# Kernel tuning notes

Measured on AMD Instinct MI355X. Metric: run time of the kernel, lower is better.

The kernel has to match this reference:

```python
import jax, jax.numpy as jnp
import numpy as np
import math

FACTOR = 1

def setup_inputs() -> dict:
    key = jax.random.key(0)
    kq, kk, kv = jax.random.split(key, 3)
    B, L, H, D = 8, 4096, 8, 32
    queries = jax.random.normal(kq, (B, L, H, D), dtype=jnp.float32)
    keys = jax.random.normal(kk, (B, L, H, D), dtype=jnp.float32)
    values = jax.random.normal(kv, (B, L, H, D), dtype=jnp.float32)
    return {"queries": queries, "keys": keys, "values": values}


def reference(queries, keys, values):
    # queries/keys/values: [B, L, H, D]
    B, L, H, D = queries.shape
    q = jnp.transpose(queries, (0, 2, 1, 3))  # [B,H,L,D]
    k = jnp.transpose(keys, (0, 2, 1, 3))
    v = jnp.transpose(values, (0, 2, 1, 3))

    # FFT-based cross-correlation (period-based dependency discovery)
    q_fft = jnp.fft.rfft(q, axis=2)
    k_fft = jnp.fft.rfft(k, axis=2)
    spd = jnp.sum(q_fft * jnp.conj(k_fft), axis=-1)      # [B,H,Lf]
    corr = jnp.fft.irfft(spd, n=L, axis=-1)              # [B,H,L]

    # Time-delay aggregation (inference path: per-sample delays)
    top_k = max(1, min(int(FACTOR * math.log(L)), L))
    weights, delays = jax.lax.top_k(corr, top_k)          # [B,H,K]
    weights = jax.nn.softmax(weights, axis=-1)

    # roll values by -delay via circular gather: pattern[l] = v[(l+delay) % L]
    init_index = jnp.arange(L)[None, None, None, :]       # [1,1,1,L]
    idx = (init_index + delays[..., None]) % L            # [B,H,K,L]
    patterns = jnp.take_along_axis(v[:, :, None, :, :], idx[..., None], axis=3)  # [B,H,K,L,D]
    agg = jnp.sum(patterns * weights[..., None, None], axis=2)  # [B,H,L,D]

    # dropout is identity in eval mode
    return jnp.transpose(agg, (0, 2, 1, 3))  # [B,L,H,D]
```

## Files before the change

kernel.cpp:

```cpp
#include <hip/hip_runtime.h>
#include <hip/hip_bf16.h>


#define SWZ(i) ((i) ^ (((i) >> 4) & 15))
#define SLICE 2056

typedef float nfloat4 __attribute__((ext_vector_type(4)));

__device__ inline void cmul(float& outr, float& outi, float ar, float ai, float br, float bi) {
    outr = ar * br - ai * bi;
    outi = ar * bi + ai * br;
}

template<int DIR>
__device__ inline void fft16(float* vr, float* vi) {
    const float C1 = 0.92387953251128675613f;
    const float S1 = 0.38268343236508977173f;
    const float R2 = 0.70710678118654752440f;
    float ur[16], ui[16];
#pragma unroll
    for (int n2 = 0; n2 < 4; ++n2) {
        float ar = vr[n2],      ai = vi[n2];
        float br = vr[n2 + 4],  bi = vi[n2 + 4];
        float cr = vr[n2 + 8],  ci = vi[n2 + 8];
        float dr = vr[n2 + 12], di = vi[n2 + 12];
        float acr = ar + cr, aci = ai + ci;
        float asr = ar - cr, asi = ai - ci;
        float bdr = br + dr, bdi = bi + di;
        float bsr = br - dr, bsi = bi - di;
        ur[0 + n2]  = acr + bdr; ui[0 + n2]  = aci + bdi;
        ur[8 + n2]  = acr - bdr; ui[8 + n2]  = aci - bdi;
        if (DIR < 0) {
            ur[4 + n2]  = asr + bsi; ui[4 + n2]  = asi - bsr;
            ur[12 + n2] = asr - bsi; ui[12 + n2] = asi + bsr;
        } else {
            ur[4 + n2]  = asr - bsi; ui[4 + n2]  = asi + bsr;
            ur[12 + n2] = asr + bsi; ui[12 + n2] = asi - bsr;
        }
    }
#pragma unroll
    for (int k1 = 1; k1 < 4; ++k1) {
#pragma unroll
        for (int n2 = 1; n2 < 4; ++n2) {
            int e = k1 * n2;
            float c, s;
            if (e == 1)      { c = C1;  s = S1; }
            else if (e == 2) { c = R2;  s = R2; }
            else if (e == 3) { c = S1;  s = C1; }
            else if (e == 4) { c = 0.f; s = 1.f; }
            else if (e == 6) { c = -R2; s = R2; }
            else             { c = -C1; s = -S1; }
            int idx = k1 * 4 + n2;
            float r0 = ur[idx], i0 = ui[idx];
            if (DIR < 0) { ur[idx] = r0 * c + i0 * s; ui[idx] = i0 * c - r0 * s; }
            else         { ur[idx] = r0 * c - i0 * s; ui[idx] = i0 * c + r0 * s; }
        }
    }
#pragma unroll
    for (int k1 = 0; k1 < 4; ++k1) {
        float ar = ur[k1 * 4 + 0], ai = ui[k1 * 4 + 0];
        float br = ur[k1 * 4 + 1], bi = ui[k1 * 4 + 1];
        float cr = ur[k1 * 4 + 2], ci = ui[k1 * 4 + 2];
        float dr = ur[k1 * 4 + 3], di = ui[k1 * 4 + 3];
        float acr = ar + cr, aci = ai + ci;
        float asr = ar - cr, asi = ai - ci;
        float bdr = br + dr, bdi = bi + di;
        float bsr = br - dr, bsi = bi - di;
        vr[k1]      = acr + bdr; vi[k1]      = aci + bdi;
        vr[k1 + 8]  = acr - bdr; vi[k1 + 8]  = aci - bdi;
        if (DIR < 0) {
            vr[k1 + 4]  = asr + bsi; vi[k1 + 4]  = asi - bsr;
            vr[k1 + 12] = asr - bsi; vi[k1 + 12] = asi + bsr;
        } else {
            vr[k1 + 4]  = asr - bsi; vi[k1 + 4]  = asi + bsr;
            vr[k1 + 12] = asr + bsi; vi[k1 + 12] = asi - bsr;
        }
    }
}

template<int DIR, int NS>
__device__ inline void fft_pass16_ip(float2* __restrict__ buf,
                                     float w1r, float w1i, int j) {
    float vr[16], vi[16];
#pragma unroll
    for (int r = 0; r < 16; ++r) {
        float2 x = buf[SWZ(j + r * 256)];
        vr[r] = x.x; vi[r] = x.y;
    }
    if (NS > 1) {
        float wr[16], wi[16];
        wr[1] = w1r; wi[1] = w1i;
#pragma unroll
        for (int r = 2; r < 16; ++r)
            cmul(wr[r], wi[r], wr[r >> 1], wi[r >> 1], wr[(r + 1) >> 1], wi[(r + 1) >> 1]);
#pragma unroll
        for (int r = 1; r < 16; ++r) {
            float r0 = vr[r], i0 = vi[r];
            vr[r] = r0 * wr[r] - i0 * wi[r];
            vi[r] = r0 * wi[r] + i0 * wr[r];
        }
    }
    fft16<DIR>(vr, vi);
    __syncthreads();
    int base = (j / NS) * (16 * NS) + (j & (NS - 1));
#pragma unroll
    for (int r = 0; r < 16; ++r)
        buf[SWZ(base + r * NS)] = make_float2(vr[r], vi[r]);
}

template<int DIR>
__device__ inline void fft4096_ip(float2* buf, float c2, float s2,
                                  float c3, float s3, int tid) {
    fft_pass16_ip<DIR, 1>(buf, 1.f, 0.f, tid);  __syncthreads();
    fft_pass16_ip<DIR, 16>(buf, c2, s2, tid);   __syncthreads();
    fft_pass16_ip<DIR, 256>(buf, c3, s3, tid);  __syncthreads();
}

__global__ __launch_bounds__(256) void transpose_pack_kernel(const float4* __restrict__ q4,
                                                             const float4* __restrict__ k4,
                                                             float4* __restrict__ xT4) {
    __shared__ float qs[64][65];
    __shared__ float ks[64][65];
    int bid = blockIdx.x;
    int ct = bid & 3;
    int lt = (bid >> 2) & 63;
    int b  = bid >> 8;
    int tid = threadIdx.x;
    int l0 = lt * 64, c0 = ct * 64;
    int cw = tid & 15;
    int rr = tid >> 4;
#pragma unroll
    for (int it = 0; it < 4; ++it) {
        int row = it * 16 + rr;
        size_t g = (size_t)(b * 4096 + l0 + row) * 64u + (size_t)(c0 / 4 + cw);
        float4 qv = q4[g];
        float4 kv = k4[g];
        qs[row][cw * 4 + 0] = qv.x; qs[row][cw * 4 + 1] = qv.y;
        qs[row][cw * 4 + 2] = qv.z; qs[row][cw * 4 + 3] = qv.w;
        ks[row][cw * 4 + 0] = kv.x; ks[row][cw * 4 + 1] = kv.y;
        ks[row][cw * 4 + 2] = kv.z; ks[row][cw * 4 + 3] = kv.w;
    }
    __syncthreads();
    int a = tid & 31;
    int cb = tid >> 5;
#pragma unroll
    for (int it = 0; it < 8; ++it) {
        int cc = it * 8 + cb;
        float4 o;
        o.x = qs[2 * a][cc];     o.y = ks[2 * a][cc];
        o.z = qs[2 * a + 1][cc]; o.w = ks[2 * a + 1][cc];
        xT4[(size_t)(b * 256 + c0 + cc) * 2048u + (size_t)(l0 / 2 + a)] = o;
    }
}

__device__ inline void spd_pair_accum(const float2* A, float4* acc, float& accny, int tid) {
#pragma unroll
    for (int t = 0; t < 4; ++t) {
        int f0 = 2 * tid + 512 * t;
        float2 za = A[SWZ(f0)];
        float2 zb = A[SWZ(f0 + 1)];
        float2 ma = A[SWZ((4096 - f0) & 4095)];
        float2 mb = A[SWZ(4095 - f0)];
        float qr = za.x + ma.x, qi = za.y - ma.y;
        float kr = za.y + ma.y, ki = za.x - ma.x;
        acc[t].x += 0.25f * (qr * kr - qi * ki);
        acc[t].y += 0.25f * (qr * ki + qi * kr);
        qr = zb.x + mb.x; qi = zb.y - mb.y;
        kr = zb.y + mb.y; ki = zb.x - mb.x;
        acc[t].z += 0.25f * (qr * kr - qi * ki);
        acc[t].w += 0.25f * (qr * ki + qi * kr);
    }
    float2 zn = A[SWZ(2048)];
    accny += zn.x * zn.y;
}

__global__ __launch_bounds__(256, 4) void fwd_spd_fast(const float2* __restrict__ xT,
                                                       float2* __restrict__ spd_d) {
    __shared__ float2 A[4096];
    int bid = blockIdx.x;
    int tid = threadIdx.x;
    int b = bid >> 7, p = bid & 127;
    const float TWO_PI = 6.2831853071795864769f;
    float ang2 = TWO_PI * (float)((tid & 15) * 16) * (1.0f / 4096.0f);
    float ang3 = TWO_PI * (float)tid * (1.0f / 4096.0f);
    float c2 = cosf(ang2), s2 = sinf(ang2);
    float c3 = cosf(ang3), s3 = sinf(ang3);
    float4 acc[4];
#pragma unroll
    for (int t = 0; t < 4; ++t) acc[t] = make_float4(0.f, 0.f, 0.f, 0.f);
    float accny = 0.f;
#pragma unroll
    for (int cc = 0; cc < 2; ++cc) {
        if (cc) __syncthreads();
        const float4* src4 = (const float4*)(xT + (size_t)(b * 256 + p * 2 + cc) * 4096u);
#pragma unroll
        for (int t = 0; t < 8; ++t) {
            float4 x = src4[tid + t * 256];
            int n = 2 * (tid + t * 256);
            A[SWZ(n)]     = make_float2(x.x, x.y);
            A[SWZ(n + 1)] = make_float2(x.z, x.w);
        }
        __syncthreads();
        fft4096_ip<-1>(A, c2, -s2, c3, -s3, tid);
        spd_pair_accum(A, acc, accny, tid);
    }
    float4* dst4 = (float4*)(spd_d + (size_t)bid * SLICE);
#pragma unroll
    for (int t = 0; t < 4; ++t) dst4[tid + t * 256] = acc[t];
    if (tid == 0) spd_d[(size_t)bid * SLICE + 2048] = make_float2(accny, 0.f);
}

__global__ __launch_bounds__(256, 4) void fwd_spd_slow(const float* __restrict__ q,
                                                       const float* __restrict__ k,
                                                       float2* __restrict__ spd_d) {
    __shared__ float2 A[4096];
    int bid = blockIdx.x;
    int tid = threadIdx.x;
    int b = bid >> 7, p = bid & 127;
    const float TWO_PI = 6.2831853071795864769f;
    float ang2 = TWO_PI * (float)((tid & 15) * 16) * (1.0f / 4096.0f);
    float ang3 = TWO_PI * (float)tid * (1.0f / 4096.0f);
    float c2 = cosf(ang2), s2 = sinf(ang2);
    float c3 = cosf(ang3), s3 = sinf(ang3);
    float4 acc[4];
#pragma unroll
    for (int t = 0; t < 4; ++t) acc[t] = make_float4(0.f, 0.f, 0.f, 0.f);
    float accny = 0.f;
#pragma unroll
    for (int cc = 0; cc < 2; ++cc) {
        if (cc) __syncthreads();
        size_t base = (size_t)b * 1048576u + (size_t)(p * 2 + cc);
#pragma unroll
        for (int t = 0; t < 16; ++t) {
            int n = tid + t * 256;
            A[SWZ(n)] = make_float2(q[base + (size_t)n * 256u], k[base + (size_t)n * 256u]);
        }
        __syncthreads();
        fft4096_ip<-1>(A, c2, -s2, c3, -s3, tid);
        spd_pair_accum(A, acc, accny, tid);
    }
    float4* dst4 = (float4*)(spd_d + (size_t)bid * SLICE);
#pragma unroll
    for (int t = 0; t < 4; ++t) dst4[tid + t * 256] = acc[t];
    if (tid == 0) spd_d[(size_t)bid * SLICE + 2048] = make_float2(accny, 0.f);
}

__global__ __launch_bounds__(256, 4) void ifft_topk_kernel(const float2* __restrict__ spd_d,
                                                           float* __restrict__ wout,
                                                           int* __restrict__ dout) {
    __shared__ float2 A[4096];
    __shared__ float rv[8][4];
    __shared__ int   ri[8][4];
    int bh = blockIdx.x;
    int b = bh >> 3, h = bh & 7;
    int tid = threadIdx.x;
    const float TWO_PI = 6.2831853071795864769f;
    float ang2 = TWO_PI * (float)((tid & 15) * 16) * (1.0f / 4096.0f);
    float ang3 = TWO_PI * (float)tid * (1.0f / 4096.0f);
    float c2 = cosf(ang2), s2 = sinf(ang2);
    float c3 = cosf(ang3), s3 = sinf(ang3);
    const float sc = 1.0f / 4096.0f;
    const float2* base = spd_d + (size_t)(b * 128 + h * 16) * SLICE;
    const float4* base4 = (const float4*)base;
#pragma unroll
    for (int t = 0; t < 4; ++t) {
        int f0 = 2 * tid + 512 * t;
        float4 a = make_float4(0.f, 0.f, 0.f, 0.f);
#pragma unroll
        for (int s = 0; s < 16; ++s) {
            float4 x = base4[(size_t)s * (SLICE / 2) + (size_t)(tid + 256 * t)];
            a.x += x.x; a.y += x.y; a.z += x.z; a.w += x.w;
        }
        float r0 = a.x * sc, i0 = a.y * sc;
        float r1 = a.z * sc, i1 = a.w * sc;
        A[SWZ(f0)]     = make_float2(r0, i0);
        A[SWZ(f0 + 1)] = make_float2(r1, i1);
        if (f0 > 0) A[SWZ(4096 - f0)] = make_float2(r0, -i0);
        A[SWZ(4095 - f0)] = make_float2(r1, -i1);
    }
    if (tid == 0) {
        float ny = 0.f;
#pragma unroll
        for (int s = 0; s < 16; ++s) ny += base[(size_t)s * SLICE + 2048].x;
        A[SWZ(2048)] = make_float2(ny * sc, 0.f);
    }
    __syncthreads();
    fft4096_ip<1>(A, c2, s2, c3, s3, tid);
    float cv[16];
#pragma unroll
    for (int t = 0; t < 16; ++t) cv[t] = A[SWZ(tid + t * 256)].x;

    int lane = tid & 63, wid = tid >> 6;
    float topv[8]; int topi[8];
    for (int kk = 0; kk < 8; ++kk) {
        float best = -3.0e38f; int bi = 0;
#pragma unroll
        for (int t = 0; t < 16; ++t) {
            int f = tid + t * 256;
            if (cv[t] > best) { best = cv[t]; bi = f; }
        }
#pragma unroll
        for (int off = 32; off > 0; off >>= 1) {
            float ov = __shfl_xor(best, off, 64);
            int   oi = __shfl_xor(bi, off, 64);
            if (ov > best || (ov == best && oi < bi)) { best = ov; bi = oi; }
        }
        if (lane == 0) { rv[kk][wid] = best; ri[kk][wid] = bi; }
        __syncthreads();
        float fb = rv[kk][0]; int fi = ri[kk][0];
#pragma unroll
        for (int w = 1; w < 4; ++w) {
            float ov = rv[kk][w]; int oi = ri[kk][w];
            if (ov > fb || (ov == fb && oi < fi)) { fb = ov; fi = oi; }
        }
        topv[kk] = fb; topi[kk] = fi;
        if (tid == (fi & 255)) {
            int t_owner = fi >> 8;
#pragma unroll
            for (int t = 0; t < 16; ++t)
                if (t == t_owner) cv[t] = -3.0e38f;
        }
    }
    if (tid == 0) {
        float mx = topv[0];
        float e[8], s = 0.0f;
#pragma unroll
        for (int kk = 0; kk < 8; ++kk) { e[kk] = expf(topv[kk] - mx); s += e[kk]; }
        float inv = 1.0f / s;
#pragma unroll
        for (int kk = 0; kk < 8; ++kk) {
            wout[bh * 8 + kk] = e[kk] * inv;
            dout[bh * 8 + kk] = topi[kk];
        }
    }
}

__global__ __launch_bounds__(256) void agg_kernel(const float4* __restrict__ v4,
                                                  const float* __restrict__ w,
                                                  const int* __restrict__ dl,
                                                  float4* __restrict__ out4) {
    __shared__ float sw[64];
    __shared__ int   sd[64];
    int blk = blockIdx.x;
    int b = blk & 7, lg = blk >> 3;
    int tid = threadIdx.x;
    if (tid < 64) {
        int h = tid >> 3, kk = tid & 7;
        sw[tid] = w[(b * 8 + h) * 8 + kk];
        sd[tid] = dl[(b * 8 + h) * 8 + kk];
    }
    __syncthreads();
    int lq = tid >> 6;
    int c4 = tid & 63;
    int h  = c4 >> 3;
    float w_[8]; int d_[8];
#pragma unroll
    for (int kk = 0; kk < 8; ++kk) { w_[kk] = sw[h * 8 + kk]; d_[kk] = sd[h * 8 + kk]; }
#pragma unroll
    for (int rep = 0; rep < 4; ++rep) {
        int l = lg * 16 + rep * 4 + lq;
        float4 acc = make_float4(0.f, 0.f, 0.f, 0.f);
#pragma unroll
        for (int kk = 0; kk < 8; ++kk) {
            int l2 = (l + d_[kk]) & 4095;
            float4 x = v4[(size_t)(b * 4096 + l2) * 64u + (size_t)c4];
            acc.x += w_[kk] * x.x; acc.y += w_[kk] * x.y;
            acc.z += w_[kk] * x.z; acc.w += w_[kk] * x.w;
        }
        nfloat4 nv = {acc.x, acc.y, acc.z, acc.w};
        __builtin_nontemporal_store(nv,
            (nfloat4*)&out4[(size_t)(b * 4096 + l) * 64u + (size_t)c4]);
    }
}

extern "C" void kernel_launch(void* const* d_in, const int* in_sizes, int n_in,
                              void* d_out, int out_size, void* d_ws, size_t ws_size,
                              hipStream_t stream) {
    const float* q = (const float*)d_in[0];
    const float* k = (const float*)d_in[1];
    const float* v = (const float*)d_in[2];
    float* ws  = (float*)d_ws;
    float2* spd_d = (float2*)d_out;

    const size_t XT_FLOATS = 16777216u;
    const size_t FAST_FLOATS = XT_FLOATS + 1024u;
    bool fast = ws_size >= FAST_FLOATS * sizeof(float);

    if (fast) {
        float* wbuf = ws + XT_FLOATS;
        int*   dbuf = (int*)(wbuf + 512);
        transpose_pack_kernel<<<2048, 256, 0, stream>>>((const float4*)q, (const float4*)k,
                                                        (float4*)ws);
        fwd_spd_fast<<<1024, 256, 0, stream>>>((const float2*)ws, spd_d);
        ifft_topk_kernel<<<64, 256, 0, stream>>>(spd_d, wbuf, dbuf);
        agg_kernel<<<2048, 256, 0, stream>>>((const float4*)v, wbuf, dbuf, (float4*)d_out);
    } else {
        float* wbuf = ws;
        int*   dbuf = (int*)(wbuf + 512);
        fwd_spd_slow<<<1024, 256, 0, stream>>>(q, k, spd_d);
        ifft_topk_kernel<<<64, 256, 0, stream>>>(spd_d, wbuf, dbuf);
        agg_kernel<<<2048, 256, 0, stream>>>((const float4*)v, wbuf, dbuf, (float4*)d_out);
    }
}
```

Measured before the change: 95.28 us.

## Fuse first radix-16 FFT pass into transpose kernel

The transpose kernel now gathers strided time samples (stride 256) for each channel, performs the first radix-16 FFT stage in registers, and writes the partially transformed data. The SPD kernel then runs only the remaining two FFT passes, saving one LDS pass and a barrier per 4096-point transform. Occupancy hint for the SPD kernel is raised from 4 to 5 blocks per CU. The transpose kernel's global reads become more scattered across L, and its writes now depend on the FFT pass matching the expected in-place ordering.

```diff
diff --git a/kernel.cpp b/kernel.cpp
--- a/kernel.cpp
+++ b/kernel.cpp
@@ -116,41 +116,51 @@
     fft_pass16_ip<DIR, 256>(buf, c3, s3, tid);  __syncthreads();
 }
 
-__global__ __launch_bounds__(256) void transpose_pack_kernel(const float4* __restrict__ q4,
+template<int DIR>
+__device__ inline void fft4096_p23(float2* buf, float c2, float s2,
+                                   float c3, float s3, int tid) {
+    fft_pass16_ip<DIR, 16>(buf, c2, s2, tid);   __syncthreads();
+    fft_pass16_ip<DIR, 256>(buf, c3, s3, tid);  __syncthreads();
+}
+
+__global__ __launch_bounds__(256) void transpose_fft1_kernel(const float4* __restrict__ q4,
                                                              const float4* __restrict__ k4,
-                                                             float4* __restrict__ xT4) {
-    __shared__ float qs[64][65];
-    __shared__ float ks[64][65];
+                                                             float4* __restrict__ y4) {
+    __shared__ float2 X[64][65];
     int bid = blockIdx.x;
-    int ct = bid & 3;
-    int lt = (bid >> 2) & 63;
+    int jt = bid & 63;
+    int ct = (bid >> 6) & 3;
     int b  = bid >> 8;
     int tid = threadIdx.x;
-    int l0 = lt * 64, c0 = ct * 64;
+    int j0 = jt * 4, c0 = ct * 64;
     int cw = tid & 15;
-    int rr = tid >> 4;
+    int rb = tid >> 4;
 #pragma unroll
     for (int it = 0; it < 4; ++it) {
-        int row = it * 16 + rr;
-        size_t g = (size_t)(b * 4096 + l0 + row) * 64u + (size_t)(c0 / 4 + cw);
+        int rr = it * 16 + rb;
+        int l  = j0 + (rr & 3) + 256 * (rr >> 2);
+        size_t g = (size_t)(b * 4096 + l) * 64u + (size_t)(c0 / 4 + cw);
         float4 qv = q4[g];
         float4 kv = k4[g];
-        qs[row][cw * 4 + 0] = qv.x; qs[row][cw * 4 + 1] = qv.y;
-        qs[row][cw * 4 + 2] = qv.z; qs[row][cw * 4 + 3] = qv.w;
-        ks[row][cw * 4 + 0] = kv.x; ks[row][cw * 4 + 1] = kv.y;
-        ks[row][cw * 4 + 2] = kv.z; ks[row][cw * 4 + 3] = kv.w;
+        X[rr][cw * 4 + 0] = make_float2(qv.x, kv.x);
+        X[rr][cw * 4 + 1] = make_float2(qv.y, kv.y);
+        X[rr][cw * 4 + 2] = make_float2(qv.z, kv.z);
+        X[rr][cw * 4 + 3] = make_float2(qv.w, kv.w);
     }
     __syncthreads();
-    int a = tid & 31;
-    int cb = tid >> 5;
-#pragma unroll
-    for (int it = 0; it < 8; ++it) {
-        int cc = it * 8 + cb;
-        float4 o;
-        o.x = qs[2 * a][cc];     o.y = ks[2 * a][cc];
-        o.z = qs[2 * a + 1][cc]; o.w = ks[2 * a + 1][cc];
-        xT4[(size_t)(b * 256 + c0 + cc) * 2048u + (size_t)(l0 / 2 + a)] = o;
-    }
+    int cc = tid & 63;
+    int jj = tid >> 6;
+    float vr[16], vi[16];
+#pragma unroll
+    for (int t = 0; t < 16; ++t) {
+        float2 x = X[t * 4 + jj][cc];
+        vr[t] = x.x; vi[t] = x.y;
+    }
+    fft16<-1>(vr, vi);
+    float4* dst = y4 + (size_t)(b * 256 + c0 + cc) * 2048u + (size_t)(j0 + jj) * 8u;
+#pragma unroll
+    for (int p = 0; p < 8; ++p)
+        dst[p] = make_float4(vr[2 * p], vi[2 * p], vr[2 * p + 1], vi[2 * p + 1]);
 }
 
 __device__ inline void spd_pair_accum(const float2* A, float4* acc, float& accny, int tid) {
@@ -174,7 +184,7 @@
     accny += zn.x * zn.y;
 }
 
-__global__ __launch_bounds__(256, 4) void fwd_spd_fast(const float2* __restrict__ xT,
+__global__ __launch_bounds__(256, 5) void fwd_spd_fast(const float2* __restrict__ y,
                                                        float2* __restrict__ spd_d) {
     __shared__ float2 A[4096];
     int bid = blockIdx.x;
@@ -192,7 +202,7 @@
 #pragma unroll
     for (int cc = 0; cc < 2; ++cc) {
         if (cc) __syncthreads();
-        const float4* src4 = (const float4*)(xT + (size_t)(b * 256 + p * 2 + cc) * 4096u);
+        const float4* src4 = (const float4*)(y + (size_t)(b * 256 + p * 2 + cc) * 4096u);
 #pragma unroll
         for (int t = 0; t < 8; ++t) {
             float4 x = src4[tid + t * 256];
@@ -201,7 +211,7 @@
             A[SWZ(n + 1)] = make_float2(x.z, x.w);
         }
         __syncthreads();
-        fft4096_ip<-1>(A, c2, -s2, c3, -s3, tid);
+        fft4096_p23<-1>(A, c2, -s2, c3, -s3, tid);
         spd_pair_accum(A, acc, accny, tid);
     }
     float4* dst4 = (float4*)(spd_d + (size_t)bid * SLICE);
@@ -382,14 +392,14 @@
     float* ws  = (float*)d_ws;
     float2* spd_d = (float2*)d_out;
 
-    const size_t XT_FLOATS = 16777216u;
-    const size_t FAST_FLOATS = XT_FLOATS + 1024u;
+    const size_t Y_FLOATS = 16777216u;
+    const size_t FAST_FLOATS = Y_FLOATS + 1024u;
     bool fast = ws_size >= FAST_FLOATS * sizeof(float);
 
     if (fast) {
-        float* wbuf = ws + XT_FLOATS;
+        float* wbuf = ws + Y_FLOATS;
         int*   dbuf = (int*)(wbuf + 512);
-        transpose_pack_kernel<<<2048, 256, 0, stream>>>((const float4*)q, (const float4*)k,
+        transpose_fft1_kernel<<<2048, 256, 0, stream>>>((const float4*)q, (const float4*)k,
                                                         (float4*)ws);
         fwd_spd_fast<<<1024, 256, 0, stream>>>((const float2*)ws, spd_d);
         ifft_topk_kernel<<<64, 256, 0, stream>>>(spd_d, wbuf, dbuf);
```

Measured after the change: 189.8 us. 99.2% more time.
